# Optimization experiments

Measured on AMD Instinct MI355X. Metric: run time of the kernel, lower is better.

## Reference

```python
import jax, jax.numpy as jnp
import numpy as np

EMBED = 1024
HEADS = 16
INTERNAL = 1024  # embedding_dim // downsample_rate
HEAD_DIM = INTERNAL // HEADS


def setup_inputs() -> dict:
    key = jax.random.key(0)
    ks = jax.random.split(key, 12)
    B, S = 2, 2048
    s_in = 1.0 / np.sqrt(EMBED)
    s_out = 1.0 / np.sqrt(INTERNAL)
    return {
        "queries": jax.random.normal(ks[0], (B, S, EMBED), jnp.float32),
        "keys": jax.random.normal(ks[1], (B, S, EMBED), jnp.float32),
        "values": jax.random.normal(ks[2], (B, S, EMBED), jnp.float32),
        "Wq": jax.random.uniform(ks[3], (EMBED, INTERNAL), jnp.float32, -s_in, s_in),
        "bq": jax.random.uniform(ks[4], (INTERNAL,), jnp.float32, -s_in, s_in),
        "Wk": jax.random.uniform(ks[5], (EMBED, INTERNAL), jnp.float32, -s_in, s_in),
        "bk": jax.random.uniform(ks[6], (INTERNAL,), jnp.float32, -s_in, s_in),
        "Wv": jax.random.uniform(ks[7], (EMBED, INTERNAL), jnp.float32, -s_in, s_in),
        "bv": jax.random.uniform(ks[8], (INTERNAL,), jnp.float32, -s_in, s_in),
        "Wo": jax.random.uniform(ks[9], (INTERNAL, EMBED), jnp.float32, -s_out, s_out),
        "bo": jax.random.uniform(ks[10], (EMBED,), jnp.float32, -s_out, s_out),
    }


def _split_heads(x):
    B, S, D = x.shape
    return x.reshape(B, S, HEADS, D // HEADS).transpose(0, 2, 1, 3)  # bhsd


def reference(queries, keys, values, Wq, bq, Wk, bk, Wv, bv, Wo, bo):
    q = _split_heads(queries @ Wq + bq)
    k = _split_heads(keys @ Wk + bk)
    v = _split_heads(values @ Wv + bv)
    # NOTE: original scales by 1/sqrt(internal_dim), not 1/sqrt(head_dim)
    scale = 1.0 / np.sqrt(INTERNAL).astype(np.float32)
    scores = jnp.einsum("bhqd,bhkd->bhqk", q, k) * scale
    probs = jax.nn.softmax(scores, axis=-1)
    out = jnp.einsum("bhqk,bhkd->bhqd", probs, v)
    B, H, S, Dh = out.shape
    out = out.transpose(0, 2, 1, 3).reshape(B, S, H * Dh)
    return out @ Wo + bo
```

## Files before the change

### kernel.cpp

```cpp
#include <hip/hip_runtime.h>
#include <stdint.h>

typedef unsigned short u16;
typedef __attribute__((ext_vector_type(8))) short short8;
typedef __attribute__((ext_vector_type(4))) float f32x4;
typedef __attribute__((ext_vector_type(16))) float f32x16;
typedef __attribute__((ext_vector_type(8))) unsigned short u16x8;
typedef __attribute__((ext_vector_type(4))) unsigned short u16x4;
typedef __attribute__((ext_vector_type(4))) uint32_t u32x4;

#if __has_builtin(__builtin_amdgcn_exp2f)
#define EXP2(x) __builtin_amdgcn_exp2f(x)
#else
#define EXP2(x) exp2f(x)
#endif

__device__ __forceinline__ u16 f2bf(float f) {
  union { float f; uint32_t u; } v; v.f = f;
  uint32_t r = (v.u + 0x7FFFu + ((v.u >> 16) & 1u)) >> 16;
  return (u16)r;
}

__device__ __forceinline__ uint32_t pack2(float a, float b) {
  return (__float_as_uint(b) & 0xffff0000u) | (__float_as_uint(a) >> 16);
}

__device__ __forceinline__ void gload_lds16(const void* g, void* l) {
  __builtin_amdgcn_global_load_lds(
      (const __attribute__((address_space(1))) void*)g,
      (__attribute__((address_space(3))) void*)l,
      16, 0, 0);
}

__global__ __launch_bounds__(256) void cvt_x(const float* __restrict__ q,
                                             const float* __restrict__ k,
                                             const float* __restrict__ v,
                                             u16* __restrict__ dst) {
  const float* src = blockIdx.z == 0 ? q : (blockIdx.z == 1 ? k : v);
  u16* d = dst + (size_t)blockIdx.z * (4096u * 1024u);
  size_t i = ((size_t)blockIdx.x * 256 + threadIdx.x) * 8;
  float4 a = *(const float4*)(src + i);
  float4 b = *(const float4*)(src + i + 4);
  u16x8 o;
  o[0] = f2bf(a.x); o[1] = f2bf(a.y); o[2] = f2bf(a.z); o[3] = f2bf(a.w);
  o[4] = f2bf(b.x); o[5] = f2bf(b.y); o[6] = f2bf(b.z); o[7] = f2bf(b.w);
  *(u16x8*)(d + i) = o;
}

__global__ __launch_bounds__(256) void cvt_wt(const float* __restrict__ Wq,
                                              const float* __restrict__ Wk,
                                              const float* __restrict__ Wv,
                                              const float* __restrict__ Wo,
                                              u16* __restrict__ Wt4) {
  const float* W = blockIdx.z == 0 ? Wq : (blockIdx.z == 1 ? Wk
                   : (blockIdx.z == 2 ? Wv : Wo));
  u16* Wt = Wt4 + (size_t)blockIdx.z * (1024u * 1024u);
  __shared__ u16 tile[64][65];
  int kt = blockIdx.x * 64, nt = blockIdx.y * 64;
  int t = threadIdx.x;
#pragma unroll
  for (int r = 0; r < 4; ++r) {
    int id = t + r * 256;
    int kk = id >> 4, c4 = id & 15;
    float4 vv = *(const float4*)(W + (size_t)(kt + kk) * 1024 + nt + c4 * 4);
    tile[kk][c4 * 4 + 0] = f2bf(vv.x);
    tile[kk][c4 * 4 + 1] = f2bf(vv.y);
    tile[kk][c4 * 4 + 2] = f2bf(vv.z);
    tile[kk][c4 * 4 + 3] = f2bf(vv.w);
  }
  __syncthreads();
#pragma unroll
  for (int r = 0; r < 4; ++r) {
    int id = t + r * 256;
    int n = id >> 4, kc = id & 15;
    u16x4 o;
    o[0] = tile[kc * 4 + 0][n];
    o[1] = tile[kc * 4 + 1][n];
    o[2] = tile[kc * 4 + 2][n];
    o[3] = tile[kc * 4 + 3][n];
    *(u16x4*)(Wt + (size_t)(nt + n) * 1024 + kt + kc * 4) = o;
  }
}

template <bool F32OUT>
__device__ __forceinline__ void gemm_tile(const u16* __restrict__ A,
                                          const u16* __restrict__ Bt,
                                          const float* __restrict__ bias,
                                          u16* __restrict__ Cb,
                                          float* __restrict__ Cf,
                                          float scale, int bm, int bn) {
  __shared__ u16 Alds[128 * 64];
  __shared__ u16 Blds[128 * 64];
  const int tid = threadIdx.x;
  const int lane = tid & 63, w = tid >> 6;
  const int wm = (w >> 1) * 64, wn = (w & 1) * 64;
  const int l15 = lane & 15, lg = lane >> 4;

  f32x4 acc[4][4] = {};

  int srow[4], scol[4], soff[4];
#pragma unroll
  for (int i = 0; i < 4; ++i) {
    int o = (w * 4 + i) * 1024 + lane * 16;
    int row = o >> 7;
    int kc = ((o >> 4) & 7) ^ (row & 7);
    srow[i] = row; scol[i] = kc * 8; soff[i] = o;
  }

  for (int kt = 0; kt < 16; ++kt) {
    __syncthreads();
#pragma unroll
    for (int i = 0; i < 4; ++i) {
      gload_lds16(A + (size_t)(bm * 128 + srow[i]) * 1024 + kt * 64 + scol[i],
                  (char*)Alds + soff[i]);
      gload_lds16(Bt + (size_t)(bn * 128 + srow[i]) * 1024 + kt * 64 + scol[i],
                  (char*)Blds + soff[i]);
    }
    __syncthreads();
#pragma unroll
    for (int ks = 0; ks < 2; ++ks) {
      short8 af[4], bf[4];
#pragma unroll
      for (int m = 0; m < 4; ++m) {
        int r = wm + m * 16 + l15;
        int byt = r * 128 + ((ks * 64 + lg * 16) ^ ((r & 7) << 4));
        af[m] = *(const short8*)((const char*)Alds + byt);
      }
#pragma unroll
      for (int n = 0; n < 4; ++n) {
        int r = wn + n * 16 + l15;
        int byt = r * 128 + ((ks * 64 + lg * 16) ^ ((r & 7) << 4));
        bf[n] = *(const short8*)((const char*)Blds + byt);
      }
#pragma unroll
      for (int m = 0; m < 4; ++m)
#pragma unroll
        for (int n = 0; n < 4; ++n)
          acc[m][n] = __builtin_amdgcn_mfma_f32_16x16x32_bf16(
              af[m], bf[n], acc[m][n], 0, 0, 0);
    }
  }
#pragma unroll
  for (int m = 0; m < 4; ++m) {
    int row0 = bm * 128 + wm + m * 16 + lg * 4;
#pragma unroll
    for (int n = 0; n < 4; ++n) {
      int col = bn * 128 + wn + n * 16 + l15;
      float bvv = bias[col];
#pragma unroll
      for (int r = 0; r < 4; ++r) {
        float v = (acc[m][n][r] + bvv) * scale;
        if (F32OUT)
          Cf[(size_t)(row0 + r) * 1024 + col] = v;
        else
          Cb[(size_t)(row0 + r) * 1024 + col] = f2bf(v);
      }
    }
  }
}

__global__ __launch_bounds__(256) void proj_kernel(const u16* __restrict__ X3,
                                                   const u16* __restrict__ Wt3,
                                                   const float* __restrict__ bq,
                                                   const float* __restrict__ bk,
                                                   const float* __restrict__ bv,
                                                   u16* __restrict__ out3) {
  int z = blockIdx.z;
  const float* bias = z == 0 ? bq : (z == 1 ? bk : bv);
  float scale = z == 0 ? 0.045084220f : 1.0f;
  gemm_tile<false>(X3 + (size_t)z * 4096 * 1024, Wt3 + (size_t)z * 1024 * 1024,
                   bias, out3 + (size_t)z * 4096 * 1024, nullptr, scale,
                   blockIdx.x, blockIdx.y);
}

__global__ __launch_bounds__(256) void outproj_kernel(const u16* __restrict__ Att,
                                                      const u16* __restrict__ Wot,
                                                      const float* __restrict__ bo,
                                                      float* __restrict__ out) {
  gemm_tile<true>(Att, Wot, bo, nullptr, out, 1.0f, blockIdx.x, blockIdx.y);
}

__global__ __launch_bounds__(256) void vt_kernel(const u16* __restrict__ v,
                                                 u16* __restrict__ vt) {
  int bh = blockIdx.y;
  int sbase = blockIdx.x * 64;
  int b = bh >> 4, h = bh & 15;
  __shared__ u16 tile[64][65];
  int t = threadIdx.x;
#pragma unroll
  for (int r = 0; r < 2; ++r) {
    int id = t + r * 256;
    int s = id >> 3, dc = id & 7;
    u16x8 x = *(const u16x8*)(v + (size_t)(b * 2048 + sbase + s) * 1024 +
                              h * 64 + dc * 8);
#pragma unroll
    for (int j = 0; j < 8; ++j) tile[s][dc * 8 + j] = x[j];
  }
  __syncthreads();
#pragma unroll
  for (int r = 0; r < 2; ++r) {
    int id = t + r * 256;
    int d = id >> 3, sc = id & 7;
    u16x8 o;
#pragma unroll
    for (int j = 0; j < 8; ++j) o[j] = tile[sc * 8 + j][d];
    *(u16x8*)(vt + ((size_t)bh * 64 + d) * 2048 + sbase + sc * 8) = o;
  }
}

__global__ __launch_bounds__(256, 1) void attn_kernel(const u16* __restrict__ q,
                                                      const u16* __restrict__ k,
                                                      const u16* __restrict__ vt,
                                                      u16* __restrict__ att) {
  __shared__ u16 smem[16384];
  const int tid = threadIdx.x, lane = tid & 63, w = tid >> 6;
  const int l31 = lane & 31, hi = lane >> 5;
  const int bh = blockIdx.y, b = bh >> 4, h = bh & 15;
  const int qb = blockIdx.x * 256 + w * 64;

  short8 qf[2][4];
#pragma unroll
  for (int g = 0; g < 2; ++g) {
    const u16* qrow =
        q + (size_t)(b * 2048 + qb + g * 32 + l31) * 1024 + h * 64 + hi * 8;
#pragma unroll
    for (int s = 0; s < 4; ++s) qf[g][s] = *(const short8*)(qrow + s * 16);
  }

  f32x16 acc[2][2] = {};
  float lsum[2] = {0.f, 0.f};

  int scol[2], rowK[2], rowV[2];
#pragma unroll
  for (int i = 0; i < 2; ++i) {
    int gi = i * 256 + tid;
    int row = gi & 63, c16 = gi >> 6;
    scol[i] = c16 * 8;
    rowV[i] = row;
    rowK[i] = row ^ ((((row >> 2) ^ (row >> 3)) & 1) ? 12 : 0);
  }
  const u16* ksrc = k + (size_t)b * 2048 * 1024 + h * 64;
  const u16* vsrc = vt + (size_t)bh * 64 * 2048;

#pragma unroll
  for (int i = 0; i < 2; ++i) {
    gload_lds16(ksrc + (size_t)rowK[i] * 1024 + scol[i],
                (char*)smem + i * 4096 + tid * 16);
    gload_lds16(vsrc + (size_t)rowV[i] * 2048 + scol[i],
                (char*)smem + 8192 + i * 4096 + tid * 16);
  }

  for (int t = 0; t < 32; ++t) {
    const int cur = t & 1;
    __syncthreads();
    if (t + 1 < 32) {
      char* dst = (char*)smem + (cur ^ 1) * 16384;
      const int kb2 = (t + 1) * 64;
#pragma unroll
      for (int i = 0; i < 2; ++i) {
        gload_lds16(ksrc + (size_t)(kb2 + rowK[i]) * 1024 + scol[i],
                    dst + i * 4096 + tid * 16);
        gload_lds16(vsrc + (size_t)rowV[i] * 2048 + kb2 + scol[i],
                    dst + 8192 + i * 4096 + tid * 16);
      }
    }
    const char* KL = (const char*)smem + cur * 16384;
    const char* VL = KL + 8192;

#pragma unroll
    for (int kg = 0; kg < 2; ++kg) {
      short8 ak[4], bv[4];
#pragma unroll
      for (int s = 0; s < 4; ++s)
        ak[s] = *(const short8*)(KL + (s * 2 + hi) * 1024 +
                                 (kg * 32 + l31) * 16);
#pragma unroll
      for (int c = 0; c < 2; ++c)
#pragma unroll
        for (int half = 0; half < 2; ++half)
          bv[c * 2 + half] =
              *(const short8*)(VL + (kg * 4 + c * 2 + hi) * 1024 +
                               (half * 32 + l31) * 16);
#pragma unroll
      for (int g = 0; g < 2; ++g) {
        f32x16 sc = {};
#pragma unroll
        for (int s = 0; s < 4; ++s)
          sc = __builtin_amdgcn_mfma_f32_32x32x16_bf16(ak[s], qf[g][s], sc,
                                                       0, 0, 0);
        float p[16];
#pragma unroll
        for (int e = 0; e < 16; ++e) p[e] = EXP2(sc[e]);
#pragma unroll
        for (int e = 0; e < 16; e += 4)
          lsum[g] += (p[e] + p[e + 1]) + (p[e + 2] + p[e + 3]);
#pragma unroll
        for (int c = 0; c < 2; ++c) {
          u32x4 fw;
          fw[0] = pack2(p[8 * c + 0], p[8 * c + 1]);
          fw[1] = pack2(p[8 * c + 2], p[8 * c + 3]);
          fw[2] = pack2(p[8 * c + 4], p[8 * c + 5]);
          fw[3] = pack2(p[8 * c + 6], p[8 * c + 7]);
          short8 pf = __builtin_bit_cast(short8, fw);
          acc[g][0] = __builtin_amdgcn_mfma_f32_32x32x16_bf16(
              pf, bv[c * 2 + 0], acc[g][0], 0, 0, 0);
          acc[g][1] = __builtin_amdgcn_mfma_f32_32x32x16_bf16(
              pf, bv[c * 2 + 1], acc[g][1], 0, 0, 0);
        }
      }
    }
  }

  float rinv[2];
#pragma unroll
  for (int g = 0; g < 2; ++g) {
    float ltot = lsum[g] + __shfl_xor(lsum[g], 32);
    rinv[g] = 1.0f / ltot;
  }
  __syncthreads();
  u16* tw = smem + w * 4096;
#pragma unroll
  for (int g = 0; g < 2; ++g)
#pragma unroll
    for (int r = 0; r < 16; ++r) {
      int rq = (r & 3) + 8 * (r >> 2) + 4 * hi;
      float ri = __shfl(rinv[g], rq);
      int row = g * 32 + rq;
      tw[row * 64 + l31] = (u16)(__float_as_uint(acc[g][0][r] * ri) >> 16);
      tw[row * 64 + 32 + l31] = (u16)(__float_as_uint(acc[g][1][r] * ri) >> 16);
    }
  asm volatile("s_waitcnt lgkmcnt(0)" ::: "memory");
  __builtin_amdgcn_sched_barrier(0);
  u16* abase = att + (size_t)(b * 2048 + qb) * 1024 + h * 64;
#pragma unroll
  for (int i = 0; i < 8; ++i) {
    int id = lane + i * 64;
    int row = id >> 3, ch = id & 7;
    u16x8 vv = *(const u16x8*)(tw + row * 64 + ch * 8);
    *(u16x8*)(abase + (size_t)row * 1024 + ch * 8) = vv;
  }
}

extern "C" void kernel_launch(void* const* d_in, const int* in_sizes, int n_in,
                              void* d_out, int out_size, void* d_ws,
                              size_t ws_size, hipStream_t stream) {
  const float* Q  = (const float*)d_in[0];
  const float* K  = (const float*)d_in[1];
  const float* V  = (const float*)d_in[2];
  const float* Wq = (const float*)d_in[3];
  const float* bq = (const float*)d_in[4];
  const float* Wk = (const float*)d_in[5];
  const float* bk = (const float*)d_in[6];
  const float* Wv = (const float*)d_in[7];
  const float* bv = (const float*)d_in[8];
  const float* Wo = (const float*)d_in[9];
  const float* bo = (const float*)d_in[10];
  float* out = (float*)d_out;

  u16* ws = (u16*)d_ws;
  const size_t SZX = (size_t)4096 * 1024;
  const size_t SZW = (size_t)1024 * 1024;
  u16* Xbf   = ws;
  u16* Wtbf  = ws + 3 * SZX;
  u16* QKVbf = Wtbf + 4 * SZW;
  u16* VTbf  = QKVbf + 3 * SZX;
  u16* ATTbf = VTbf + SZX;

  hipLaunchKernelGGL(cvt_x, dim3(2048, 1, 3), dim3(256), 0, stream, Q, K, V,
                     Xbf);
  hipLaunchKernelGGL(cvt_wt, dim3(16, 16, 4), dim3(256), 0, stream, Wq, Wk, Wv,
                     Wo, Wtbf);
  hipLaunchKernelGGL(proj_kernel, dim3(32, 8, 3), dim3(256), 0, stream, Xbf,
                     Wtbf, bq, bk, bv, QKVbf);
  hipLaunchKernelGGL(vt_kernel, dim3(32, 32), dim3(256), 0, stream,
                     QKVbf + 2 * SZX, VTbf);
  hipLaunchKernelGGL(attn_kernel, dim3(8, 32), dim3(256), 0, stream, QKVbf,
                     QKVbf + SZX, VTbf, ATTbf);
  hipLaunchKernelGGL(outproj_kernel, dim3(32, 8), dim3(256), 0, stream, ATTbf,
                     Wtbf + 3 * SZW, bo, out);
}
```

Measured before the change: 126.9 us.

## Split attention KV range across two blocks and merge partial outputs

The attention grid gains a z dimension that splits the 2048-key range in half. Each block writes unnormalized bf16 partial outputs and per-row exp sums into workspace reused from the no-longer-needed converted inputs. A new merge kernel adds the two partials and normalizes by the combined sum. Launch bounds go to 2 blocks per CU, so twice as many blocks fill the GPU and hide latency better. The cost is an extra kernel launch, extra global memory traffic for partials and an extra bf16 rounding step.

```diff
diff --git a/kernel.cpp b/kernel.cpp
--- a/kernel.cpp
+++ b/kernel.cpp
@@ -19,6 +19,11 @@
   union { float f; uint32_t u; } v; v.f = f;
   uint32_t r = (v.u + 0x7FFFu + ((v.u >> 16) & 1u)) >> 16;
   return (u16)r;
+}
+
+__device__ __forceinline__ float bf2f(u16 u) {
+  union { uint32_t u; float f; } v; v.u = ((uint32_t)u) << 16;
+  return v.f;
 }
 
 __device__ __forceinline__ uint32_t pack2(float a, float b) {
@@ -208,14 +213,16 @@
   }
 }
 
-__global__ __launch_bounds__(256, 1) void attn_kernel(const u16* __restrict__ q,
+__global__ __launch_bounds__(256, 2) void attn_kernel(const u16* __restrict__ q,
                                                       const u16* __restrict__ k,
                                                       const u16* __restrict__ vt,
-                                                      u16* __restrict__ att) {
+                                                      u16* __restrict__ attp,
+                                                      float* __restrict__ lp) {
   __shared__ u16 smem[16384];
   const int tid = threadIdx.x, lane = tid & 63, w = tid >> 6;
   const int l31 = lane & 31, hi = lane >> 5;
   const int bh = blockIdx.y, b = bh >> 4, h = bh & 15;
+  const int z = blockIdx.z;
   const int qb = blockIdx.x * 256 + w * 64;
 
   short8 qf[2][4];
@@ -241,21 +248,22 @@
   }
   const u16* ksrc = k + (size_t)b * 2048 * 1024 + h * 64;
   const u16* vsrc = vt + (size_t)bh * 64 * 2048;
+  const int kb0 = z * 1024;
 
 #pragma unroll
   for (int i = 0; i < 2; ++i) {
-    gload_lds16(ksrc + (size_t)rowK[i] * 1024 + scol[i],
+    gload_lds16(ksrc + (size_t)(kb0 + rowK[i]) * 1024 + scol[i],
                 (char*)smem + i * 4096 + tid * 16);
-    gload_lds16(vsrc + (size_t)rowV[i] * 2048 + scol[i],
+    gload_lds16(vsrc + (size_t)rowV[i] * 2048 + kb0 + scol[i],
                 (char*)smem + 8192 + i * 4096 + tid * 16);
   }
 
-  for (int t = 0; t < 32; ++t) {
-    const int cur = t & 1;
+  for (int tt = 0; tt < 16; ++tt) {
+    const int cur = tt & 1;
     __syncthreads();
-    if (t + 1 < 32) {
+    if (tt + 1 < 16) {
       char* dst = (char*)smem + (cur ^ 1) * 16384;
-      const int kb2 = (t + 1) * 64;
+      const int kb2 = kb0 + (tt + 1) * 64;
 #pragma unroll
       for (int i = 0; i < 2; ++i) {
         gload_lds16(ksrc + (size_t)(kb2 + rowK[i]) * 1024 + scol[i],
@@ -311,12 +319,16 @@
     }
   }
 
-  float rinv[2];
-#pragma unroll
-  for (int g = 0; g < 2; ++g) {
-    float ltot = lsum[g] + __shfl_xor(lsum[g], 32);
-    rinv[g] = 1.0f / ltot;
-  }
+  float lt[2];
+#pragma unroll
+  for (int g = 0; g < 2; ++g) lt[g] = lsum[g] + __shfl_xor(lsum[g], 32);
+  if (hi == 0) {
+    float* lbase = lp + (size_t)z * 65536;
+#pragma unroll
+    for (int g = 0; g < 2; ++g)
+      lbase[(size_t)(b * 2048 + qb + g * 32 + l31) * 16 + h] = lt[g];
+  }
+
   __syncthreads();
   u16* tw = smem + w * 4096;
 #pragma unroll
@@ -324,14 +336,14 @@
 #pragma unroll
     for (int r = 0; r < 16; ++r) {
       int rq = (r & 3) + 8 * (r >> 2) + 4 * hi;
-      float ri = __shfl(rinv[g], rq);
       int row = g * 32 + rq;
-      tw[row * 64 + l31] = (u16)(__float_as_uint(acc[g][0][r] * ri) >> 16);
-      tw[row * 64 + 32 + l31] = (u16)(__float_as_uint(acc[g][1][r] * ri) >> 16);
+      tw[row * 64 + l31] = f2bf(acc[g][0][r]);
+      tw[row * 64 + 32 + l31] = f2bf(acc[g][1][r]);
     }
   asm volatile("s_waitcnt lgkmcnt(0)" ::: "memory");
   __builtin_amdgcn_sched_barrier(0);
-  u16* abase = att + (size_t)(b * 2048 + qb) * 1024 + h * 64;
+  u16* abase = attp + (size_t)z * (4096u * 1024u) +
+               (size_t)(b * 2048 + qb) * 1024 + h * 64;
 #pragma unroll
   for (int i = 0; i < 8; ++i) {
     int id = lane + i * 64;
@@ -339,6 +351,24 @@
     u16x8 vv = *(const u16x8*)(tw + row * 64 + ch * 8);
     *(u16x8*)(abase + (size_t)row * 1024 + ch * 8) = vv;
   }
+}
+
+__global__ __launch_bounds__(256) void merge_kernel(const u16* __restrict__ a0,
+                                                    const u16* __restrict__ a1,
+                                                    const float* __restrict__ lp,
+                                                    u16* __restrict__ out) {
+  size_t i0 = ((size_t)blockIdx.x * 256 + threadIdx.x) * 8;
+  int row = (int)(i0 >> 10);
+  int head = (int)((i0 >> 6) & 15);
+  float l = lp[(size_t)row * 16 + head] + lp[65536 + (size_t)row * 16 + head];
+  float rinv = 1.0f / l;
+  u16x8 x0 = *(const u16x8*)(a0 + i0);
+  u16x8 x1 = *(const u16x8*)(a1 + i0);
+  u16x8 o;
+#pragma unroll
+  for (int j = 0; j < 8; ++j)
+    o[j] = f2bf((bf2f(x0[j]) + bf2f(x1[j])) * rinv);
+  *(u16x8*)(out + i0) = o;
 }
 
 extern "C" void kernel_launch(void* const* d_in, const int* in_sizes, int n_in,
@@ -365,6 +395,8 @@
   u16* QKVbf = Wtbf + 4 * SZW;
   u16* VTbf  = QKVbf + 3 * SZX;
   u16* ATTbf = VTbf + SZX;
+  u16*   attP  = Xbf;
+  float* lsumP = (float*)(Xbf + 2 * SZX);
 
   hipLaunchKernelGGL(cvt_x, dim3(2048, 1, 3), dim3(256), 0, stream, Q, K, V,
                      Xbf);
@@ -374,8 +406,10 @@
                      Wtbf, bq, bk, bv, QKVbf);
   hipLaunchKernelGGL(vt_kernel, dim3(32, 32), dim3(256), 0, stream,
                      QKVbf + 2 * SZX, VTbf);
-  hipLaunchKernelGGL(attn_kernel, dim3(8, 32), dim3(256), 0, stream, QKVbf,
-                     QKVbf + SZX, VTbf, ATTbf);
+  hipLaunchKernelGGL(attn_kernel, dim3(8, 32, 2), dim3(256), 0, stream, QKVbf,
+                     QKVbf + SZX, VTbf, attP, lsumP);
+  hipLaunchKernelGGL(merge_kernel, dim3(2048), dim3(256), 0, stream, attP,
+                     attP + SZX, lsumP, ATTbf);
   hipLaunchKernelGGL(outproj_kernel, dim3(32, 8), dim3(256), 0, stream, ATTbf,
                      Wtbf + 3 * SZW, bo, out);
 }
```

Measured after the change: 123.4 us. 2.7% less time.
